# Kernel optimization log

Measured on AMD Instinct MI355X. Metric: run time of the kernel, lower is better.

Reference implementation:

```python
import jax, jax.numpy as jnp
import numpy as np

D_K = 16  # fixed by module globals
N_HEADS = 1

def setup_inputs() -> dict:
    key = jax.random.key(0)
    ks = jax.random.split(key, 7)
    B, H, S, d = 4, N_HEADS, 4096, D_K
    Q = jax.random.normal(ks[0], (B, H, S, d), dtype=jnp.float32)
    K = jax.random.normal(ks[1], (B, H, S, d), dtype=jnp.float32)
    V = jax.random.normal(ks[2], (B, H, S, d), dtype=jnp.float32)
    attn_mask = jax.random.randint(ks[3], (B, H, S, S), 0, 2).astype(jnp.bool_)
    link_sim_mat = jax.random.uniform(ks[4], (B, S, S), dtype=jnp.float32)
    # 1x1 Conv2d(1->1) params: a single scalar weight and scalar bias
    sim_w = jax.random.normal(ks[5], (), dtype=jnp.float32) * 0.5
    sim_b = jax.random.normal(ks[6], (), dtype=jnp.float32) * 0.1
    return {"Q": Q, "K": K, "V": V, "attn_mask": attn_mask,
            "link_sim_mat": link_sim_mat, "sim_w": sim_w, "sim_b": sim_b}

def reference(Q, K, V, attn_mask, link_sim_mat, sim_w, sim_b):
    # scores = QK^T / sqrt(d_k)  -> [B,H,S,S]
    scores = jnp.einsum('bhqd,bhkd->bhqk', Q, K) / jnp.sqrt(jnp.float32(D_K))
    # 1x1 conv on [B,1,S,S] with 1 in/out channel == scalar affine
    sim_link = sim_w * link_sim_mat + sim_b          # [B,S,S]
    scores = scores + sim_link[:, None, :, :]        # broadcast over heads
    scores = jnp.where(attn_mask, jnp.float32(-1e9), scores)
    attn = jax.nn.softmax(scores, axis=-1)
    context = jnp.einsum('bhqk,bhkd->bhqd', attn, V)
    return (context, attn)
```

## Files before the change

### kernel.cpp

```cpp
#include <hip/hip_runtime.h>

#define SS    4096
#define DK    16
#define NB    4
#define TQ    4
#define BLOCK 256
#define KPT   16

__global__ void detect_mask_dtype(const unsigned* __restrict__ m,
                                  int* __restrict__ flag)
{
    unsigned acc = 0;
    for (int i = 0; i < 1024; ++i) acc |= m[i];
    *flag = (acc > 1u) ? 1 : 0;
}

__global__ __launch_bounds__(BLOCK)
void attn_fused(const float* __restrict__ Qm, const float* __restrict__ Km,
                const float* __restrict__ Vm, const void*  __restrict__ Mraw,
                const float* __restrict__ Lm, const float* __restrict__ WP,
                const float* __restrict__ BP, const int*   __restrict__ flagp,
                float* __restrict__ Co, float* __restrict__ Ao)
{
    __shared__ float redl[4][TQ];
    __shared__ float redc[4][TQ][DK];

    const int tid = threadIdx.x;
    const int b   = blockIdx.x >> 10;
    const int q0  = (blockIdx.x & 1023) * TQ;

    const bool  m8 = (*flagp != 0);
    const float sw = WP[0];
    const float sb = BP[0];

    const float* qp = Qm + ((size_t)b * SS + q0) * DK;
    const float* kp = Km + (size_t)b * SS * DK;
    const float* vp = Vm + (size_t)b * SS * DK;
    const size_t mrow = (size_t)b * SS * SS + (size_t)q0 * SS;
    const int*           mp32 = (const int*)Mraw           + mrow;
    const unsigned char* mp8  = (const unsigned char*)Mraw + mrow;
    const float* lp = Lm + mrow;
    float*       ap = Ao + mrow;

    float qreg[TQ][DK];
    #pragma unroll
    for (int qq = 0; qq < TQ; ++qq)
        #pragma unroll
        for (int d = 0; d < DK; ++d)
            qreg[qq][d] = __uint_as_float(
                __builtin_amdgcn_readfirstlane(__float_as_uint(qp[qq * DK + d])));

    const int k0 = tid * KPT;

    float p[TQ][KPT];
    float lsum[TQ] = {0.f, 0.f, 0.f, 0.f};

    #pragma unroll
    for (int j = 0; j < KPT / 4; ++j) {
        int4     mi[TQ];
        unsigned mu[TQ];
        float4   li[TQ];
        if (m8) {
            #pragma unroll
            for (int qq = 0; qq < TQ; ++qq)
                mu[qq] = *(const unsigned*)(mp8 + (size_t)qq * SS + k0 + 4 * j);
        } else {
            #pragma unroll
            for (int qq = 0; qq < TQ; ++qq)
                mi[qq] = *(const int4*)(mp32 + (size_t)qq * SS + k0 + 4 * j);
        }
        #pragma unroll
        for (int qq = 0; qq < TQ; ++qq)
            li[qq] = *(const float4*)(lp + (size_t)qq * SS + k0 + 4 * j);

        #pragma unroll
        for (int u = 0; u < 4; ++u) {
            const int i = 4 * j + u;
            const int k = k0 + i;
            const float4 ka = *(const float4*)(kp + (size_t)k * DK + 0);
            const float4 kb = *(const float4*)(kp + (size_t)k * DK + 4);
            const float4 kc = *(const float4*)(kp + (size_t)k * DK + 8);
            const float4 kd = *(const float4*)(kp + (size_t)k * DK + 12);
            const float kr[DK] = {ka.x, ka.y, ka.z, ka.w,
                                  kb.x, kb.y, kb.z, kb.w,
                                  kc.x, kc.y, kc.z, kc.w,
                                  kd.x, kd.y, kd.z, kd.w};
            #pragma unroll
            for (int qq = 0; qq < TQ; ++qq) {
                float s = 0.f;
                #pragma unroll
                for (int d = 0; d < DK; ++d)
                    s = fmaf(qreg[qq][d], kr[d], s);
                const float lv = (u == 0) ? li[qq].x : (u == 1) ? li[qq].y
                                : (u == 2) ? li[qq].z : li[qq].w;
                const int mv = m8
                    ? (int)((mu[qq] >> (8 * u)) & 0xffu)
                    : ((u == 0) ? mi[qq].x : (u == 1) ? mi[qq].y
                     : (u == 2) ? mi[qq].z : mi[qq].w);
                s = s * 0.25f + fmaf(sw, lv, sb);
                const float e  = __expf(s);
                const float pv = mv ? 0.f : e;
                p[qq][i] = pv;
                lsum[qq] += pv;
            }
        }
    }

    const int lane = tid & 63;
    const int wv   = tid >> 6;
    #pragma unroll
    for (int qq = 0; qq < TQ; ++qq) {
        float v = lsum[qq];
        #pragma unroll
        for (int off = 32; off; off >>= 1)
            v += __shfl_down(v, off);
        lsum[qq] = v;
    }
    if (lane == 0) {
        #pragma unroll
        for (int qq = 0; qq < TQ; ++qq)
            redl[wv][qq] = lsum[qq];
    }
    __syncthreads();
    float rl[TQ];
    #pragma unroll
    for (int qq = 0; qq < TQ; ++qq)
        rl[qq] = 1.0f / (redl[0][qq] + redl[1][qq] + redl[2][qq] + redl[3][qq]);

    float ctx[TQ][DK];
    #pragma unroll
    for (int qq = 0; qq < TQ; ++qq)
        #pragma unroll
        for (int d = 0; d < DK; ++d)
            ctx[qq][d] = 0.f;

    #pragma unroll
    for (int i = 0; i < KPT; ++i) {
        const int k = k0 + i;
        const float4 va = *(const float4*)(vp + (size_t)k * DK + 0);
        const float4 vb = *(const float4*)(vp + (size_t)k * DK + 4);
        const float4 vc = *(const float4*)(vp + (size_t)k * DK + 8);
        const float4 vd = *(const float4*)(vp + (size_t)k * DK + 12);
        const float vr[DK] = {va.x, va.y, va.z, va.w,
                              vb.x, vb.y, vb.z, vb.w,
                              vc.x, vc.y, vc.z, vc.w,
                              vd.x, vd.y, vd.z, vd.w};
        #pragma unroll
        for (int qq = 0; qq < TQ; ++qq) {
            const float pn = p[qq][i] * rl[qq];
            p[qq][i] = pn;
            #pragma unroll
            for (int d = 0; d < DK; ++d)
                ctx[qq][d] = fmaf(pn, vr[d], ctx[qq][d]);
        }
    }

    #pragma unroll
    for (int qq = 0; qq < TQ; ++qq)
        #pragma unroll
        for (int j = 0; j < KPT / 4; ++j) {
            float4 st = {p[qq][4 * j + 0], p[qq][4 * j + 1],
                         p[qq][4 * j + 2], p[qq][4 * j + 3]};
            *(float4*)(ap + (size_t)qq * SS + k0 + 4 * j) = st;
        }

    #pragma unroll
    for (int qq = 0; qq < TQ; ++qq)
        #pragma unroll
        for (int d = 0; d < DK; ++d) {
            float v = ctx[qq][d];
            #pragma unroll
            for (int off = 32; off; off >>= 1)
                v += __shfl_down(v, off);
            ctx[qq][d] = v;
        }
    if (lane == 0) {
        #pragma unroll
        for (int qq = 0; qq < TQ; ++qq)
            #pragma unroll
            for (int d = 0; d < DK; ++d)
                redc[wv][qq][d] = ctx[qq][d];
    }
    __syncthreads();
    if (tid < TQ * DK) {
        const int qq = tid >> 4;
        const int d  = tid & 15;
        const float v = redc[0][qq][d] + redc[1][qq][d]
                      + redc[2][qq][d] + redc[3][qq][d];
        Co[((size_t)b * SS + q0 + qq) * DK + d] = v;
    }
}

extern "C" void kernel_launch(void* const* d_in, const int* in_sizes, int n_in,
                              void* d_out, int out_size, void* d_ws, size_t ws_size,
                              hipStream_t stream)
{
    (void)in_sizes; (void)n_in; (void)ws_size; (void)out_size;

    const float* Q  = (const float*)d_in[0];
    const float* K  = (const float*)d_in[1];
    const float* V  = (const float*)d_in[2];
    const void*  M  = d_in[3];
    const float* L  = (const float*)d_in[4];
    const float* W  = (const float*)d_in[5];
    const float* Bp = (const float*)d_in[6];

    int* flag = (int*)d_ws;

    float* Co = (float*)d_out;
    float* Ao = (float*)d_out + (size_t)NB * SS * DK;

    detect_mask_dtype<<<1, 1, 0, stream>>>((const unsigned*)M, flag);

    dim3 grid(NB * SS / TQ);
    dim3 block(BLOCK);
    attn_fused<<<grid, block, 0, stream>>>(Q, K, V, M, L, W, Bp, flag, Co, Ao);
}
```

Before: 975.3 us.

## Transpose K/V to dim-major layout and interleave key chunks across threads

Adds a pre-pass that transposes K and V into a [B, d, S] workspace layout, so each thread reads contiguous float4s per head-dimension with coalesced access across lanes. Key columns are now split into four interleaved chunks of 1024 instead of one contiguous 16-key span per thread. Each block handles two query rows instead of four. The context accumulation is folded into the score loop, with normalization applied at the end. This aims to cut strided K/V loads and make mask, link and attention traffic coalesce better. In exchange it adds an extra kernel launch, needs workspace, and doubles the number of blocks, which re-reads K and V more often.

Result: slower. 2.154 ms (+120.8%).

```diff
diff --git a/kernel.cpp b/kernel.cpp
--- a/kernel.cpp
+++ b/kernel.cpp
@@ -3,8 +3,10 @@
 #define SS    4096
 #define DK    16
 #define NB    4
-#define TQ    4
+#define TQ    2
 #define BLOCK 256
+#define CHUNK 1024
+#define NCH   4
 #define KPT   16
 
 __global__ void detect_mask_dtype(const unsigned* __restrict__ m,
@@ -15,33 +17,64 @@
     *flag = (acc > 1u) ? 1 : 0;
 }
 
-__global__ __launch_bounds__(BLOCK)
+__global__ __launch_bounds__(256)
+void transpose_kv(const float* __restrict__ K, const float* __restrict__ V,
+                  float* __restrict__ KT, float* __restrict__ VT)
+{
+    const int t = blockIdx.x * blockDim.x + threadIdx.x;
+    const int b = t >> 12;
+    const int s = t & (SS - 1);
+
+    const float4* kp = (const float4*)(K + (size_t)t * DK);
+    const float4* vp = (const float4*)(V + (size_t)t * DK);
+    const float4 ka = kp[0], kb = kp[1], kc = kp[2], kd = kp[3];
+    const float4 va = vp[0], vb = vp[1], vc = vp[2], vd = vp[3];
+    const float kr[DK] = {ka.x, ka.y, ka.z, ka.w, kb.x, kb.y, kb.z, kb.w,
+                          kc.x, kc.y, kc.z, kc.w, kd.x, kd.y, kd.z, kd.w};
+    const float vr[DK] = {va.x, va.y, va.z, va.w, vb.x, vb.y, vb.z, vb.w,
+                          vc.x, vc.y, vc.z, vc.w, vd.x, vd.y, vd.z, vd.w};
+
+    float* ko = KT + (size_t)b * DK * SS + s;
+    float* vo = VT + (size_t)b * DK * SS + s;
+    #pragma unroll
+    for (int d = 0; d < DK; ++d) {
+        ko[(size_t)d * SS] = kr[d];
+        vo[(size_t)d * SS] = vr[d];
+    }
+}
+
+template<bool TR>
+__global__ __launch_bounds__(BLOCK, 4)
 void attn_fused(const float* __restrict__ Qm, const float* __restrict__ Km,
                 const float* __restrict__ Vm, const void*  __restrict__ Mraw,
                 const float* __restrict__ Lm, const float* __restrict__ WP,
                 const float* __restrict__ BP, const int*   __restrict__ flagp,
+                const float* __restrict__ KTp, const float* __restrict__ VTp,
                 float* __restrict__ Co, float* __restrict__ Ao)
 {
     __shared__ float redl[4][TQ];
     __shared__ float redc[4][TQ][DK];
 
     const int tid = threadIdx.x;
-    const int b   = blockIdx.x >> 10;
-    const int q0  = (blockIdx.x & 1023) * TQ;
+    const int b   = blockIdx.x >> 11;
+    const int q0  = (blockIdx.x & 2047) * TQ;
 
     const bool  m8 = (*flagp != 0);
     const float sw = WP[0];
     const float sb = BP[0];
 
     const float* qp = Qm + ((size_t)b * SS + q0) * DK;
-    const float* kp = Km + (size_t)b * SS * DK;
-    const float* vp = Vm + (size_t)b * SS * DK;
     const size_t mrow = (size_t)b * SS * SS + (size_t)q0 * SS;
     const int*           mp32 = (const int*)Mraw           + mrow;
     const unsigned char* mp8  = (const unsigned char*)Mraw + mrow;
     const float* lp = Lm + mrow;
     float*       ap = Ao + mrow;
 
+    const float* kt = KTp + (size_t)b * DK * SS;
+    const float* vt = VTp + (size_t)b * DK * SS;
+    const float* kp = Km  + (size_t)b * SS * DK;
+    const float* vp = Vm  + (size_t)b * SS * DK;
+
     float qreg[TQ][DK];
     #pragma unroll
     for (int qq = 0; qq < TQ; ++qq)
@@ -50,58 +83,125 @@
             qreg[qq][d] = __uint_as_float(
                 __builtin_amdgcn_readfirstlane(__float_as_uint(qp[qq * DK + d])));
 
-    const int k0 = tid * KPT;
+    const int kb4 = tid * 4;
 
     float p[TQ][KPT];
-    float lsum[TQ] = {0.f, 0.f, 0.f, 0.f};
-
-    #pragma unroll
-    for (int j = 0; j < KPT / 4; ++j) {
+    float lsum[TQ] = {0.f, 0.f};
+    float ctx[TQ][DK];
+    #pragma unroll
+    for (int qq = 0; qq < TQ; ++qq)
+        #pragma unroll
+        for (int d = 0; d < DK; ++d)
+            ctx[qq][d] = 0.f;
+
+    #pragma unroll
+    for (int c = 0; c < NCH; ++c) {
+        const int k0 = c * CHUNK + kb4;
+
+        float4 li[TQ];
+        #pragma unroll
+        for (int qq = 0; qq < TQ; ++qq)
+            li[qq] = *(const float4*)(lp + (size_t)qq * SS + k0);
+
+        unsigned mu[TQ];
         int4     mi[TQ];
-        unsigned mu[TQ];
-        float4   li[TQ];
         if (m8) {
             #pragma unroll
             for (int qq = 0; qq < TQ; ++qq)
-                mu[qq] = *(const unsigned*)(mp8 + (size_t)qq * SS + k0 + 4 * j);
+                mu[qq] = *(const unsigned*)(mp8 + (size_t)qq * SS + k0);
         } else {
             #pragma unroll
             for (int qq = 0; qq < TQ; ++qq)
-                mi[qq] = *(const int4*)(mp32 + (size_t)qq * SS + k0 + 4 * j);
-        }
+                mi[qq] = *(const int4*)(mp32 + (size_t)qq * SS + k0);
+        }
+
+        float s[TQ][4];
         #pragma unroll
         for (int qq = 0; qq < TQ; ++qq)
-            li[qq] = *(const float4*)(lp + (size_t)qq * SS + k0 + 4 * j);
-
-        #pragma unroll
-        for (int u = 0; u < 4; ++u) {
-            const int i = 4 * j + u;
-            const int k = k0 + i;
-            const float4 ka = *(const float4*)(kp + (size_t)k * DK + 0);
-            const float4 kb = *(const float4*)(kp + (size_t)k * DK + 4);
-            const float4 kc = *(const float4*)(kp + (size_t)k * DK + 8);
-            const float4 kd = *(const float4*)(kp + (size_t)k * DK + 12);
-            const float kr[DK] = {ka.x, ka.y, ka.z, ka.w,
-                                  kb.x, kb.y, kb.z, kb.w,
-                                  kc.x, kc.y, kc.z, kc.w,
-                                  kd.x, kd.y, kd.z, kd.w};
+            s[qq][0] = s[qq][1] = s[qq][2] = s[qq][3] = 0.f;
+
+        if (TR) {
+            #pragma unroll
+            for (int d = 0; d < DK; ++d) {
+                const float4 k4 = *(const float4*)(kt + (size_t)d * SS + k0);
+                #pragma unroll
+                for (int qq = 0; qq < TQ; ++qq) {
+                    const float q = qreg[qq][d];
+                    s[qq][0] = fmaf(q, k4.x, s[qq][0]);
+                    s[qq][1] = fmaf(q, k4.y, s[qq][1]);
+                    s[qq][2] = fmaf(q, k4.z, s[qq][2]);
+                    s[qq][3] = fmaf(q, k4.w, s[qq][3]);
+                }
+            }
+        } else {
+            #pragma unroll
+            for (int u = 0; u < 4; ++u) {
+                const int k = k0 + u;
+                const float4 ka = *(const float4*)(kp + (size_t)k * DK + 0);
+                const float4 kb = *(const float4*)(kp + (size_t)k * DK + 4);
+                const float4 kc = *(const float4*)(kp + (size_t)k * DK + 8);
+                const float4 kd = *(const float4*)(kp + (size_t)k * DK + 12);
+                const float kr[DK] = {ka.x, ka.y, ka.z, ka.w, kb.x, kb.y, kb.z, kb.w,
+                                      kc.x, kc.y, kc.z, kc.w, kd.x, kd.y, kd.z, kd.w};
+                #pragma unroll
+                for (int qq = 0; qq < TQ; ++qq) {
+                    float acc = 0.f;
+                    #pragma unroll
+                    for (int d = 0; d < DK; ++d)
+                        acc = fmaf(qreg[qq][d], kr[d], acc);
+                    s[qq][u] = acc;
+                }
+            }
+        }
+
+        float pc[TQ][4];
+        #pragma unroll
+        for (int u = 0; u < 4; ++u)
             #pragma unroll
             for (int qq = 0; qq < TQ; ++qq) {
-                float s = 0.f;
-                #pragma unroll
-                for (int d = 0; d < DK; ++d)
-                    s = fmaf(qreg[qq][d], kr[d], s);
                 const float lv = (u == 0) ? li[qq].x : (u == 1) ? li[qq].y
-                                : (u == 2) ? li[qq].z : li[qq].w;
+                               : (u == 2) ? li[qq].z : li[qq].w;
                 const int mv = m8
                     ? (int)((mu[qq] >> (8 * u)) & 0xffu)
                     : ((u == 0) ? mi[qq].x : (u == 1) ? mi[qq].y
                      : (u == 2) ? mi[qq].z : mi[qq].w);
-                s = s * 0.25f + fmaf(sw, lv, sb);
-                const float e  = __expf(s);
+                const float sv = fmaf(s[qq][u], 0.25f, fmaf(sw, lv, sb));
+                const float e  = __expf(sv);
                 const float pv = mv ? 0.f : e;
-                p[qq][i] = pv;
+                pc[qq][u]      = pv;
+                p[qq][4 * c + u] = pv;
                 lsum[qq] += pv;
+            }
+
+        if (TR) {
+            #pragma unroll
+            for (int d = 0; d < DK; ++d) {
+                const float4 v4 = *(const float4*)(vt + (size_t)d * SS + k0);
+                #pragma unroll
+                for (int qq = 0; qq < TQ; ++qq) {
+                    float a = ctx[qq][d];
+                    a = fmaf(pc[qq][0], v4.x, a);
+                    a = fmaf(pc[qq][1], v4.y, a);
+                    a = fmaf(pc[qq][2], v4.z, a);
+                    a = fmaf(pc[qq][3], v4.w, a);
+                    ctx[qq][d] = a;
+                }
+            }
+        } else {
+            #pragma unroll
+            for (int u = 0; u < 4; ++u) {
+                const int k = k0 + u;
+                const float4 va = *(const float4*)(vp + (size_t)k * DK + 0);
+                const float4 vb = *(const float4*)(vp + (size_t)k * DK + 4);
+                const float4 vc = *(const float4*)(vp + (size_t)k * DK + 8);
+                const float4 vd = *(const float4*)(vp + (size_t)k * DK + 12);
+                const float vr[DK] = {va.x, va.y, va.z, va.w, vb.x, vb.y, vb.z, vb.w,
+                                      vc.x, vc.y, vc.z, vc.w, vd.x, vd.y, vd.z, vd.w};
+                #pragma unroll
+                for (int qq = 0; qq < TQ; ++qq)
+                    #pragma unroll
+                    for (int d = 0; d < DK; ++d)
+                        ctx[qq][d] = fmaf(pc[qq][u], vr[d], ctx[qq][d]);
             }
         }
     }
@@ -127,48 +227,22 @@
     for (int qq = 0; qq < TQ; ++qq)
         rl[qq] = 1.0f / (redl[0][qq] + redl[1][qq] + redl[2][qq] + redl[3][qq]);
 
-    float ctx[TQ][DK];
+    #pragma unroll
+    for (int qq = 0; qq < TQ; ++qq) {
+        const float r = rl[qq];
+        #pragma unroll
+        for (int c = 0; c < NCH; ++c) {
+            float4 st = {p[qq][4 * c + 0] * r, p[qq][4 * c + 1] * r,
+                         p[qq][4 * c + 2] * r, p[qq][4 * c + 3] * r};
+            *(float4*)(ap + (size_t)qq * SS + c * CHUNK + kb4) = st;
+        }
+    }
+
     #pragma unroll
     for (int qq = 0; qq < TQ; ++qq)
         #pragma unroll
-        for (int d = 0; d < DK; ++d)
-            ctx[qq][d] = 0.f;
-
-    #pragma unroll
-    for (int i = 0; i < KPT; ++i) {
-        const int k = k0 + i;
-        const float4 va = *(const float4*)(vp + (size_t)k * DK + 0);
-        const float4 vb = *(const float4*)(vp + (size_t)k * DK + 4);
-        const float4 vc = *(const float4*)(vp + (size_t)k * DK + 8);
-        const float4 vd = *(const float4*)(vp + (size_t)k * DK + 12);
-        const float vr[DK] = {va.x, va.y, va.z, va.w,
-                              vb.x, vb.y, vb.z, vb.w,
-                              vc.x, vc.y, vc.z, vc.w,
-                              vd.x, vd.y, vd.z, vd.w};
-        #pragma unroll
-        for (int qq = 0; qq < TQ; ++qq) {
-            const float pn = p[qq][i] * rl[qq];
-            p[qq][i] = pn;
-            #pragma unroll
-            for (int d = 0; d < DK; ++d)
-                ctx[qq][d] = fmaf(pn, vr[d], ctx[qq][d]);
-        }
-    }
-
-    #pragma unroll
-    for (int qq = 0; qq < TQ; ++qq)
-        #pragma unroll
-        for (int j = 0; j < KPT / 4; ++j) {
-            float4 st = {p[qq][4 * j + 0], p[qq][4 * j + 1],
-                         p[qq][4 * j + 2], p[qq][4 * j + 3]};
-            *(float4*)(ap + (size_t)qq * SS + k0 + 4 * j) = st;
-        }
-
-    #pragma unroll
-    for (int qq = 0; qq < TQ; ++qq)
-        #pragma unroll
         for (int d = 0; d < DK; ++d) {
-            float v = ctx[qq][d];
+            float v = ctx[qq][d] * rl[qq];
             #pragma unroll
             for (int off = 32; off; off >>= 1)
                 v += __shfl_down(v, off);
@@ -195,7 +269,7 @@
                               void* d_out, int out_size, void* d_ws, size_t ws_size,
                               hipStream_t stream)
 {
-    (void)in_sizes; (void)n_in; (void)ws_size; (void)out_size;
+    (void)in_sizes; (void)n_in; (void)out_size;
 
     const float* Q  = (const float*)d_in[0];
     const float* K  = (const float*)d_in[1];
@@ -205,7 +279,11 @@
     const float* W  = (const float*)d_in[5];
     const float* Bp = (const float*)d_in[6];
 
-    int* flag = (int*)d_ws;
+    int*   flag = (int*)d_ws;
+    float* KT   = (float*)((char*)d_ws + 256);
+    float* VT   = KT + (size_t)NB * DK * SS;
+    const size_t need = 256 + 2ull * NB * DK * SS * sizeof(float);
+    const bool tr = (ws_size >= need);
 
     float* Co = (float*)d_out;
     float* Ao = (float*)d_out + (size_t)NB * SS * DK;
@@ -214,5 +292,12 @@
 
     dim3 grid(NB * SS / TQ);
     dim3 block(BLOCK);
-    attn_fused<<<grid, block, 0, stream>>>(Q, K, V, M, L, W, Bp, flag, Co, Ao);
+    if (tr) {
+        transpose_kv<<<dim3(NB * SS / 256), dim3(256), 0, stream>>>(K, V, KT, VT);
+        attn_fused<true><<<grid, block, 0, stream>>>(Q, K, V, M, L, W, Bp, flag,
+                                                     KT, VT, Co, Ao);
+    } else {
+        attn_fused<false><<<grid, block, 0, stream>>>(Q, K, V, M, L, W, Bp, flag,
+                                                      KT, VT, Co, Ao);
+    }
 }
```
